# Kernel optimization log

Measured on AMD Instinct MI355X. Metric: run time of the kernel, lower is better.

## Reference

```python
import jax, jax.numpy as jnp
import numpy as np

V = 50000        # output_size (vocab)
H = 1024         # internal hidden = hidden_size*2
L = 400          # max_length (encoder length)
B = 64
OOV_PAD = 500


def setup_inputs() -> dict:
    key = jax.random.key(0)
    ks = jax.random.split(key, 16)
    s = 0.02
    inp = {
        "input_ids": jax.random.randint(ks[0], (B,), 0, V),
        "hidden": jax.random.normal(ks[1], (1, B, H), jnp.float32),
        "encoder_outputs": jax.random.normal(ks[2], (L, B, H), jnp.float32),
        "full_input": jax.random.randint(ks[3], (B, L), 0, V),
        # parameters
        "emb": jax.random.normal(ks[4], (V, H), jnp.float32) * s,
        "attn_W": jax.random.normal(ks[5], (L, 2 * H), jnp.float32) * s,
        "attn_b": jnp.zeros((L,), jnp.float32),
        "comb_W": jax.random.normal(ks[6], (H, 2 * H), jnp.float32) * s,
        "comb_b": jnp.zeros((H,), jnp.float32),
        "W_ih": jax.random.normal(ks[7], (3 * H, H), jnp.float32) * s,
        "W_hh": jax.random.normal(ks[8], (3 * H, H), jnp.float32) * s,
        "b_ih": jnp.zeros((3 * H,), jnp.float32),
        "b_hh": jnp.zeros((3 * H,), jnp.float32),
        "out_W": jax.random.normal(ks[9], (V, H), jnp.float32) * s,
        "out_b": jnp.zeros((V,), jnp.float32),
        "gen_W": jax.random.normal(ks[10], (1, 2 * H), jnp.float32) * s,
        "gen_b": jnp.zeros((1,), jnp.float32),
    }
    return inp


def _decoder_step(input_ids, hidden, encoder_outputs, full_input,
                  emb, attn_W, attn_b, comb_W, comb_b,
                  W_ih, W_hh, b_ih, b_hh, out_W, out_b, gen_W, gen_b):
    embedded = emb[input_ids]                      # [B,H] (dropout is eval-mode identity)
    h0 = hidden[0]                                 # [B,H]

    # attention over fixed max_length positions
    cat = jnp.concatenate([embedded, h0], axis=1)  # [B,2H]
    attn_weights = jax.nn.softmax(cat @ attn_W.T + attn_b, axis=1)  # [B,L]
    enc = jnp.transpose(encoder_outputs, (1, 0, 2))                 # [B,L,H]
    attn_applied = jnp.einsum('bl,blh->bh', attn_weights, enc)      # [B,H]

    combined = jnp.concatenate([embedded, attn_applied], axis=1) @ comb_W.T + comb_b  # [B,H]

    # single-step GRU (PyTorch gate layout: r, z, n)
    gi = combined @ W_ih.T + b_ih
    gh = h0 @ W_hh.T + b_hh
    ir, iz, inn = jnp.split(gi, 3, axis=1)
    hr, hz, hn = jnp.split(gh, 3, axis=1)
    r = jax.nn.sigmoid(ir + hr)
    z = jax.nn.sigmoid(iz + hz)
    n = jnp.tanh(inn + r * hn)
    h_new = (1.0 - z) * n + z * h0                 # gru_output[0]

    p_vocab = jax.nn.log_softmax(h_new @ out_W.T + out_b, axis=1)   # [B,V]

    gen_in = jnp.concatenate([combined, h0], axis=1)                # [B,2H]
    p_gen = jax.nn.sigmoid(gen_in @ gen_W.T + gen_b)                # [B,1]

    # pointer copy distribution via scatter-add into [B, V+500]
    token_dist = jnp.zeros((input_ids.shape[0], V + OOV_PAD), p_vocab.dtype)
    rows = jnp.arange(input_ids.shape[0])[:, None]                  # [B,1]
    token_dist = token_dist.at[rows, full_input].add(attn_weights)

    p_vocab_scaled = p_vocab * p_gen
    padded = jnp.concatenate(
        [p_vocab_scaled, jnp.zeros((input_ids.shape[0], OOV_PAD), p_vocab.dtype)], axis=1)
    p_final = padded + (1.0 - p_gen) * token_dist
    # original module returns the INPUT hidden (not gru_hidden)
    return p_final, hidden, attn_weights


def reference(input_ids, hidden, encoder_outputs, full_input,
              emb, attn_W, attn_b, comb_W, comb_b,
              W_ih, W_hh, b_ih, b_hh, out_W, out_b, gen_W, gen_b):
    return _decoder_step(input_ids, hidden, encoder_outputs, full_input,
                         emb, attn_W, attn_b, comb_W, comb_b,
                         W_ih, W_hh, b_ih, b_hh, out_W, out_b, gen_W, gen_b)
```

## Files before the change

### kernel.cpp

```cpp
#include <hip/hip_runtime.h>
#include <cstddef>

#define B_ 64
#define H_ 1024
#define L_ 400
#define V_ 50000
#define VP_ 50500

typedef short short8 __attribute__((ext_vector_type(8)));
typedef float f32x4 __attribute__((ext_vector_type(4)));

static __device__ __forceinline__ short f2bf(float f) {
  unsigned u = __float_as_uint(f);
  u += 0x7fffu + ((u >> 16) & 1u);
  return (short)(u >> 16);
}

static __device__ __forceinline__ short8 pack8(float4 a, float4 b) {
  short8 r;
  r[0] = f2bf(a.x); r[1] = f2bf(a.y); r[2] = f2bf(a.z); r[3] = f2bf(a.w);
  r[4] = f2bf(b.x); r[5] = f2bf(b.y); r[6] = f2bf(b.z); r[7] = f2bf(b.w);
  return r;
}

__global__ void k_prep(const int* __restrict__ ids, const float* __restrict__ emb,
                       const float* __restrict__ hid, float* __restrict__ E,
                       float* __restrict__ A, float* __restrict__ hid_out) {
  int b = blockIdx.x;
  int t = threadIdx.x;
  int row = ids[b];
  float4 v = ((const float4*)(emb + (size_t)row * H_))[t];
  ((float4*)(E + (size_t)b * H_))[t] = v;
  ((float4*)(A + (size_t)b * H_))[t] = make_float4(0.f, 0.f, 0.f, 0.f);
  ((float4*)(hid_out + (size_t)b * H_))[t] = ((const float4*)(hid + (size_t)b * H_))[t];
}

__global__ __launch_bounds__(256) void k_gemm_small(
    const float* __restrict__ W0, const float* __restrict__ bias0,
    const float* __restrict__ Xa0, const float* __restrict__ Xb0,
    float* __restrict__ out0, int N0, int K0, int ldo0,
    const float* __restrict__ W1, const float* __restrict__ bias1,
    const float* __restrict__ Xa1, const float* __restrict__ Xb1,
    float* __restrict__ out1, int N1, int K1, int ldo1) {
  const float* W  = blockIdx.y ? W1  : W0;
  const float* bias = blockIdx.y ? bias1 : bias0;
  const float* Xa = blockIdx.y ? Xa1 : Xa0;
  const float* Xb = blockIdx.y ? Xb1 : Xb0;
  float* out = blockIdx.y ? out1 : out0;
  int N = blockIdx.y ? N1 : N0;
  int K = blockIdx.y ? K1 : K0;
  int ldo = blockIdx.y ? ldo1 : ldo0;

  int tid = threadIdx.x, wave = tid >> 6, lane = tid & 63;
  int q = lane >> 4, nl = lane & 15;
  int n = blockIdx.x * 16 + nl;
  int nld = n < N ? n : (N - 1);
  int kpw = K >> 2;
  int kbeg = wave * kpw;
  const float* wr = W + (size_t)nld * K;

  f32x4 acc[4];
  #pragma unroll
  for (int i = 0; i < 4; ++i) acc[i] = (f32x4){0.f, 0.f, 0.f, 0.f};

  for (int k0 = kbeg; k0 < kbeg + kpw; k0 += 32) {
    int kk = k0 + q * 8;
    float4 w0 = *(const float4*)(wr + kk);
    float4 w1 = *(const float4*)(wr + kk + 4);
    short8 bf = pack8(w0, w1);
    const float* Xsel = (kk < 1024) ? Xa : Xb;
    int kx = kk & 1023;
    #pragma unroll
    for (int mt = 0; mt < 4; ++mt) {
      const float* xp = Xsel + (size_t)(mt * 16 + nl) * H_ + kx;
      float4 x0 = *(const float4*)xp;
      float4 x1 = *(const float4*)(xp + 4);
      short8 af = pack8(x0, x1);
      acc[mt] = __builtin_amdgcn_mfma_f32_16x16x32_bf16(af, bf, acc[mt], 0, 0, 0);
    }
  }

  __shared__ float red[4][64][16];
  #pragma unroll
  for (int mt = 0; mt < 4; ++mt)
    #pragma unroll
    for (int r = 0; r < 4; ++r)
      red[wave][mt * 16 + q * 4 + r][nl] = acc[mt][r];
  __syncthreads();
  for (int i = tid; i < 1024; i += 256) {
    int m = i >> 4, c = i & 15;
    int nn = blockIdx.x * 16 + c;
    if (nn < N) {
      float s = red[0][m][c] + red[1][m][c] + red[2][m][c] + red[3][m][c] + bias[nn];
      out[(size_t)m * ldo + nn] = s;
    }
  }
}

__global__ __launch_bounds__(256) void k_attnsm(
    const float* __restrict__ S, const float* __restrict__ enc,
    float* __restrict__ aw_out, float* __restrict__ A) {
  __shared__ float w[L_];
  __shared__ float red[256];
  int lc = blockIdx.x, b = blockIdx.y, t = threadIdx.x;
  float a0 = S[b * L_ + t];
  float a1 = (t < L_ - 256) ? S[b * L_ + 256 + t] : -1e30f;
  float m = fmaxf(a0, a1);
  red[t] = m; __syncthreads();
  for (int s = 128; s > 0; s >>= 1) { if (t < s) red[t] = fmaxf(red[t], red[t + s]); __syncthreads(); }
  m = red[0]; __syncthreads();
  float e0 = __expf(a0 - m);
  float e1 = (t < L_ - 256) ? __expf(a1 - m) : 0.f;
  red[t] = e0 + e1; __syncthreads();
  for (int s = 128; s > 0; s >>= 1) { if (t < s) red[t] += red[t + s]; __syncthreads(); }
  float z = red[0];
  w[t] = e0 / z;
  if (t < L_ - 256) w[256 + t] = e1 / z;
  __syncthreads();
  if (lc == 0) {
    aw_out[b * L_ + t] = w[t];
    if (t < L_ - 256) aw_out[b * L_ + 256 + t] = w[256 + t];
  }
  float4 acc = make_float4(0.f, 0.f, 0.f, 0.f);
  for (int l = lc * 25; l < lc * 25 + 25; ++l) {
    float wg = w[l];
    float4 e = ((const float4*)(enc + ((size_t)l * B_ + b) * H_))[t];
    acc.x += wg * e.x; acc.y += wg * e.y; acc.z += wg * e.z; acc.w += wg * e.w;
  }
  float* dst = A + (size_t)b * H_ + t * 4;
  atomicAdd(dst + 0, acc.x); atomicAdd(dst + 1, acc.y);
  atomicAdd(dst + 2, acc.z); atomicAdd(dst + 3, acc.w);
}

__global__ __launch_bounds__(256) void k_gru_gen(
    const float* __restrict__ gi, const float* __restrict__ gh,
    const float* __restrict__ hid, short* __restrict__ HNb,
    const float* __restrict__ C, const float* __restrict__ gW,
    const float* __restrict__ gb, float* __restrict__ PG) {
  __shared__ float red[256];
  int blk = blockIdx.x, t = threadIdx.x;
  if (blk < 256) {
    int idx = blk * 256 + t;
    int b = idx >> 10, h = idx & 1023;
    float ir = gi[b * 3072 + h], iz = gi[b * 3072 + 1024 + h], inn = gi[b * 3072 + 2048 + h];
    float hr = gh[b * 3072 + h], hz = gh[b * 3072 + 1024 + h], hn = gh[b * 3072 + 2048 + h];
    float r = 1.f / (1.f + __expf(-(ir + hr)));
    float z = 1.f / (1.f + __expf(-(iz + hz)));
    float n = tanhf(inn + r * hn);
    HNb[idx] = f2bf((1.f - z) * n + z * hid[idx]);
  } else {
    int b = blk - 256;
    float acc = 0.f;
    for (int k = t; k < 2 * H_; k += 256) {
      float x = (k < H_) ? C[b * H_ + k] : hid[b * H_ + k - H_];
      acc += x * gW[k];
    }
    red[t] = acc; __syncthreads();
    for (int s = 128; s > 0; s >>= 1) { if (t < s) red[t] += red[t + s]; __syncthreads(); }
    if (t == 0) PG[b] = 1.f / (1.f + __expf(-(red[0] + gb[0])));
  }
}

__global__ __launch_bounds__(256) void k_gemm_vocab(
    const short* __restrict__ Xb, const float* __restrict__ W,
    const float* __restrict__ bias, float* __restrict__ P) {
  int tid = threadIdx.x, wave = tid >> 6, lane = tid & 63;
  int q = lane >> 4, nl = lane & 15;
  int n = blockIdx.x * 64 + wave * 16 + nl;
  int nld = n < V_ ? n : (V_ - 1);
  const float* wr = W + (size_t)nld * H_;
  f32x4 acc[4];
  #pragma unroll
  for (int i = 0; i < 4; ++i) acc[i] = (f32x4){0.f, 0.f, 0.f, 0.f};

  for (int k0 = 0; k0 < H_; k0 += 32) {
    int kk = k0 + q * 8;
    float4 w0 = *(const float4*)(wr + kk);
    float4 w1 = *(const float4*)(wr + kk + 4);
    short8 bf = pack8(w0, w1);
    #pragma unroll
    for (int mt = 0; mt < 4; ++mt) {
      short8 af = *(const short8*)(Xb + (size_t)(mt * 16 + nl) * H_ + kk);
      acc[mt] = __builtin_amdgcn_mfma_f32_16x16x32_bf16(af, bf, acc[mt], 0, 0, 0);
    }
  }
  if (n < V_) {
    float bv = bias[n];
    #pragma unroll
    for (int mt = 0; mt < 4; ++mt)
      #pragma unroll
      for (int r = 0; r < 4; ++r)
        P[(size_t)(mt * 16 + q * 4 + r) * VP_ + n] = acc[mt][r] + bv;
  }
}

__global__ __launch_bounds__(256) void k_rowred2(const float* __restrict__ P,
                                                 float* __restrict__ MX,
                                                 float* __restrict__ SE) {
  __shared__ float red[256];
  int b = blockIdx.x >> 2, c = blockIdx.x & 3;
  int t = threadIdx.x;
  int v0 = c * 12500, v1 = v0 + 12500;
  float m = -1e30f;
  for (int v = v0 + t; v < v1; v += 256) m = fmaxf(m, P[(size_t)b * VP_ + v]);
  red[t] = m; __syncthreads();
  for (int s = 128; s > 0; s >>= 1) { if (t < s) red[t] = fmaxf(red[t], red[t + s]); __syncthreads(); }
  m = red[0]; __syncthreads();
  float sum = 0.f;
  for (int v = v0 + t; v < v1; v += 256) sum += __expf(P[(size_t)b * VP_ + v] - m);
  red[t] = sum; __syncthreads();
  for (int s = 128; s > 0; s >>= 1) { if (t < s) red[t] += red[t + s]; __syncthreads(); }
  if (t == 0) { MX[blockIdx.x] = m; SE[blockIdx.x] = red[0]; }
}

__global__ void k_final(float* __restrict__ P, const float* __restrict__ pg,
                        const float* __restrict__ MX, const float* __restrict__ SE) {
  int b = blockIdx.y;
  float m0 = MX[b * 4], m1 = MX[b * 4 + 1], m2 = MX[b * 4 + 2], m3 = MX[b * 4 + 3];
  float M = fmaxf(fmaxf(m0, m1), fmaxf(m2, m3));
  float Z = SE[b * 4] * __expf(m0 - M) + SE[b * 4 + 1] * __expf(m1 - M)
          + SE[b * 4 + 2] * __expf(m2 - M) + SE[b * 4 + 3] * __expf(m3 - M);
  float lz = M + __logf(Z);
  float g = pg[b];
  int v0 = blockIdx.x * 1024 + threadIdx.x * 4;
  if (v0 >= VP_) return;
  float4* p = (float4*)(P + (size_t)b * VP_ + v0);
  if (v0 < V_) {
    float4 x = *p;
    x.x = g * (x.x - lz); x.y = g * (x.y - lz);
    x.z = g * (x.z - lz); x.w = g * (x.w - lz);
    *p = x;
  } else {
    *p = make_float4(0.f, 0.f, 0.f, 0.f);
  }
}

__global__ void k_scatter(float* __restrict__ P, const float* __restrict__ aw,
                          const int* __restrict__ fi, const float* __restrict__ pg) {
  int b = blockIdx.x, t = threadIdx.x;
  if (t >= L_) return;
  float g = 1.f - pg[b];
  int v = fi[b * L_ + t];
  atomicAdd(P + (size_t)b * VP_ + v, g * aw[b * L_ + t]);
}

extern "C" void kernel_launch(void* const* d_in, const int* in_sizes, int n_in,
                              void* d_out, int out_size, void* d_ws, size_t ws_size,
                              hipStream_t stream) {
  const int*   ids    = (const int*)d_in[0];
  const float* hid    = (const float*)d_in[1];
  const float* enc    = (const float*)d_in[2];
  const int*   fi     = (const int*)d_in[3];
  const float* emb    = (const float*)d_in[4];
  const float* attn_W = (const float*)d_in[5];
  const float* attn_b = (const float*)d_in[6];
  const float* comb_W = (const float*)d_in[7];
  const float* comb_b = (const float*)d_in[8];
  const float* W_ih   = (const float*)d_in[9];
  const float* W_hh   = (const float*)d_in[10];
  const float* b_ih   = (const float*)d_in[11];
  const float* b_hh   = (const float*)d_in[12];
  const float* out_W  = (const float*)d_in[13];
  const float* out_b  = (const float*)d_in[14];
  const float* gen_W  = (const float*)d_in[15];
  const float* gen_b  = (const float*)d_in[16];

  float* outp    = (float*)d_out;
  float* P       = outp;
  float* hid_out = outp + (size_t)B_ * VP_;
  float* aw_out  = hid_out + B_ * H_;

  float* ws = (float*)d_ws;
  float* E   = ws;
  float* A   = E + B_ * H_;
  float* C   = A + B_ * H_;
  float* S   = C + B_ * H_;
  float* GI  = S + B_ * L_;
  float* GH  = GI + B_ * 3 * H_;
  float* PG  = GH + B_ * 3 * H_;
  float* MX  = PG + B_;
  float* SE  = MX + 256;
  short* HNb = (short*)(SE + 256);

  k_prep<<<64, 256, 0, stream>>>(ids, emb, hid, E, A, hid_out);
  k_gemm_small<<<dim3(25, 1), 256, 0, stream>>>(
      attn_W, attn_b, E, hid, S, L_, 2 * H_, L_,
      attn_W, attn_b, E, hid, S, L_, 2 * H_, L_);
  k_attnsm<<<dim3(16, 64), 256, 0, stream>>>(S, enc, aw_out, A);
  k_gemm_small<<<dim3(64, 1), 256, 0, stream>>>(
      comb_W, comb_b, E, A, C, H_, 2 * H_, H_,
      comb_W, comb_b, E, A, C, H_, 2 * H_, H_);
  k_gemm_small<<<dim3(192, 2), 256, 0, stream>>>(
      W_ih, b_ih, C, C, GI, 3 * H_, H_, 3 * H_,
      W_hh, b_hh, hid, hid, GH, 3 * H_, H_, 3 * H_);
  k_gru_gen<<<320, 256, 0, stream>>>(GI, GH, hid, HNb, C, gen_W, gen_b, PG);
  k_gemm_vocab<<<782, 256, 0, stream>>>(HNb, out_W, out_b, P);
  k_rowred2<<<256, 256, 0, stream>>>(P, MX, SE);
  k_final<<<dim3(50, 64), 256, 0, stream>>>(P, PG, MX, SE);
  k_scatter<<<64, 512, 0, stream>>>(P, aw_out, fi, PG);
}
```

Before: 609.9 us.

## Fuse embedding gather into small GEMMs and co-schedule W_hh GEMM with attention

Removes the prep kernel by gathering embedding rows directly inside the small GEMM via an index array, and uses spare blocks of the first GEMM launch to zero the attention accumulator and copy hidden out. The W_hh GEMM, which only depends on the input hidden state, now runs in the same launch as the attention-score GEMM rather than alongside W_ih later. Float-to-bf16 packing switches to the paired hardware conversion intrinsic, and the attention-apply kernel uses half as many blocks, each doing twice as many positions, which halves the atomics. The aim is fewer launches and better use of idle CUs on the small attention GEMM. The cost is extra branching in the GEMM, and the attention kernel now has less parallelism.

```diff
diff --git a/kernel.cpp b/kernel.cpp
--- a/kernel.cpp
+++ b/kernel.cpp
@@ -1,4 +1,5 @@
 #include <hip/hip_runtime.h>
+#include <hip/hip_bf16.h>
 #include <cstddef>
 
 #define B_ 64
@@ -16,49 +17,70 @@
   return (short)(u >> 16);
 }
 
+static __device__ __forceinline__ short2 cvt2(float a, float b) {
+  union { __hip_bfloat162 h; short2 s; } u;
+  u.h = __float22bfloat162_rn(float2{a, b});
+  return u.s;
+}
+
 static __device__ __forceinline__ short8 pack8(float4 a, float4 b) {
+  short2 p0 = cvt2(a.x, a.y), p1 = cvt2(a.z, a.w);
+  short2 p2 = cvt2(b.x, b.y), p3 = cvt2(b.z, b.w);
   short8 r;
-  r[0] = f2bf(a.x); r[1] = f2bf(a.y); r[2] = f2bf(a.z); r[3] = f2bf(a.w);
-  r[4] = f2bf(b.x); r[5] = f2bf(b.y); r[6] = f2bf(b.z); r[7] = f2bf(b.w);
+  r[0] = p0.x; r[1] = p0.y; r[2] = p1.x; r[3] = p1.y;
+  r[4] = p2.x; r[5] = p2.y; r[6] = p3.x; r[7] = p3.y;
   return r;
-}
-
-__global__ void k_prep(const int* __restrict__ ids, const float* __restrict__ emb,
-                       const float* __restrict__ hid, float* __restrict__ E,
-                       float* __restrict__ A, float* __restrict__ hid_out) {
-  int b = blockIdx.x;
-  int t = threadIdx.x;
-  int row = ids[b];
-  float4 v = ((const float4*)(emb + (size_t)row * H_))[t];
-  ((float4*)(E + (size_t)b * H_))[t] = v;
-  ((float4*)(A + (size_t)b * H_))[t] = make_float4(0.f, 0.f, 0.f, 0.f);
-  ((float4*)(hid_out + (size_t)b * H_))[t] = ((const float4*)(hid + (size_t)b * H_))[t];
 }
 
 __global__ __launch_bounds__(256) void k_gemm_small(
     const float* __restrict__ W0, const float* __restrict__ bias0,
     const float* __restrict__ Xa0, const float* __restrict__ Xb0,
-    float* __restrict__ out0, int N0, int K0, int ldo0,
+    const int* __restrict__ gidx0, float* __restrict__ out0,
+    int N0, int K0, int ldo0,
     const float* __restrict__ W1, const float* __restrict__ bias1,
     const float* __restrict__ Xa1, const float* __restrict__ Xb1,
-    float* __restrict__ out1, int N1, int K1, int ldo1) {
-  const float* W  = blockIdx.y ? W1  : W0;
+    const int* __restrict__ gidx1, float* __restrict__ out1,
+    int N1, int K1, int ldo1,
+    const float* __restrict__ auxHid, float* __restrict__ auxA,
+    float* __restrict__ auxHidOut) {
+  const float* W    = blockIdx.y ? W1 : W0;
   const float* bias = blockIdx.y ? bias1 : bias0;
-  const float* Xa = blockIdx.y ? Xa1 : Xa0;
-  const float* Xb = blockIdx.y ? Xb1 : Xb0;
+  const float* Xa   = blockIdx.y ? Xa1 : Xa0;
+  const float* Xb   = blockIdx.y ? Xb1 : Xb0;
+  const int* gidx   = blockIdx.y ? gidx1 : gidx0;
   float* out = blockIdx.y ? out1 : out0;
-  int N = blockIdx.y ? N1 : N0;
-  int K = blockIdx.y ? K1 : K0;
+  int N   = blockIdx.y ? N1 : N0;
+  int K   = blockIdx.y ? K1 : K0;
   int ldo = blockIdx.y ? ldo1 : ldo0;
 
   int tid = threadIdx.x, wave = tid >> 6, lane = tid & 63;
   int q = lane >> 4, nl = lane & 15;
+
+  if ((int)blockIdx.x * 16 >= N) {
+    if (auxA) {
+      int bx = blockIdx.x - (N + 15) / 16;
+      if (bx < 64) {
+        int idx = bx * 256 + tid;
+        ((float4*)auxA)[idx] = make_float4(0.f, 0.f, 0.f, 0.f);
+        ((float4*)auxHidOut)[idx] = ((const float4*)auxHid)[idx];
+      }
+    }
+    return;
+  }
+
   int n = blockIdx.x * 16 + nl;
   int nld = n < N ? n : (N - 1);
   int kpw = K >> 2;
   int kbeg = wave * kpw;
   const float* wr = W + (size_t)nld * K;
 
+  int rid[4];
+  #pragma unroll
+  for (int mt = 0; mt < 4; ++mt) {
+    int m = mt * 16 + nl;
+    rid[mt] = gidx ? gidx[m] : m;
+  }
+
   f32x4 acc[4];
   #pragma unroll
   for (int i = 0; i < 4; ++i) acc[i] = (f32x4){0.f, 0.f, 0.f, 0.f};
@@ -68,11 +90,11 @@
     float4 w0 = *(const float4*)(wr + kk);
     float4 w1 = *(const float4*)(wr + kk + 4);
     short8 bf = pack8(w0, w1);
-    const float* Xsel = (kk < 1024) ? Xa : Xb;
-    int kx = kk & 1023;
+    bool lo = kk < 1024;
     #pragma unroll
     for (int mt = 0; mt < 4; ++mt) {
-      const float* xp = Xsel + (size_t)(mt * 16 + nl) * H_ + kx;
+      const float* xp = lo ? (Xa + (size_t)rid[mt] * H_ + kk)
+                           : (Xb + (size_t)(mt * 16 + nl) * H_ + (kk - 1024));
       float4 x0 = *(const float4*)xp;
       float4 x1 = *(const float4*)(xp + 4);
       short8 af = pack8(x0, x1);
@@ -122,7 +144,7 @@
     if (t < L_ - 256) aw_out[b * L_ + 256 + t] = w[256 + t];
   }
   float4 acc = make_float4(0.f, 0.f, 0.f, 0.f);
-  for (int l = lc * 25; l < lc * 25 + 25; ++l) {
+  for (int l = lc * 50; l < lc * 50 + 50; ++l) {
     float wg = w[l];
     float4 e = ((const float4*)(enc + ((size_t)l * B_ + b) * H_))[t];
     acc.x += wg * e.x; acc.y += wg * e.y; acc.z += wg * e.z; acc.w += wg * e.w;
@@ -271,8 +293,7 @@
   float* aw_out  = hid_out + B_ * H_;
 
   float* ws = (float*)d_ws;
-  float* E   = ws;
-  float* A   = E + B_ * H_;
+  float* A   = ws;
   float* C   = A + B_ * H_;
   float* S   = C + B_ * H_;
   float* GI  = S + B_ * L_;
@@ -282,17 +303,19 @@
   float* SE  = MX + 256;
   short* HNb = (short*)(SE + 256);
 
-  k_prep<<<64, 256, 0, stream>>>(ids, emb, hid, E, A, hid_out);
-  k_gemm_small<<<dim3(25, 1), 256, 0, stream>>>(
-      attn_W, attn_b, E, hid, S, L_, 2 * H_, L_,
-      attn_W, attn_b, E, hid, S, L_, 2 * H_, L_);
-  k_attnsm<<<dim3(16, 64), 256, 0, stream>>>(S, enc, aw_out, A);
+  k_gemm_small<<<dim3(192, 2), 256, 0, stream>>>(
+      attn_W, attn_b, emb, hid, ids, S, L_, 2 * H_, L_,
+      W_hh, b_hh, hid, hid, nullptr, GH, 3 * H_, H_, 3 * H_,
+      hid, A, hid_out);
+  k_attnsm<<<dim3(8, 64), 256, 0, stream>>>(S, enc, aw_out, A);
   k_gemm_small<<<dim3(64, 1), 256, 0, stream>>>(
-      comb_W, comb_b, E, A, C, H_, 2 * H_, H_,
-      comb_W, comb_b, E, A, C, H_, 2 * H_, H_);
-  k_gemm_small<<<dim3(192, 2), 256, 0, stream>>>(
-      W_ih, b_ih, C, C, GI, 3 * H_, H_, 3 * H_,
-      W_hh, b_hh, hid, hid, GH, 3 * H_, H_, 3 * H_);
+      comb_W, comb_b, emb, A, ids, C, H_, 2 * H_, H_,
+      comb_W, comb_b, emb, A, ids, C, H_, 2 * H_, H_,
+      nullptr, nullptr, nullptr);
+  k_gemm_small<<<dim3(192, 1), 256, 0, stream>>>(
+      W_ih, b_ih, C, C, nullptr, GI, 3 * H_, H_, 3 * H_,
+      W_ih, b_ih, C, C, nullptr, GI, 3 * H_, H_, 3 * H_,
+      nullptr, nullptr, nullptr);
   k_gru_gen<<<320, 256, 0, stream>>>(GI, GH, hid, HNb, C, gen_W, gen_b, PG);
   k_gemm_vocab<<<782, 256, 0, stream>>>(HNb, out_W, out_b, P);
   k_rowred2<<<256, 256, 0, stream>>>(P, MX, SE);
```

Result: slower. 640.8 us (+5.1%).
